# Optimization experiments

Measured on AMD Instinct MI355X. Metric: run time of the kernel, lower is better.

The kernel has to match this reference:

```python
import jax, jax.numpy as jnp
import numpy as np

SHIFT = 1  # shift_direction fixed to +1 (original picks +/-1 randomly at init)


def setup_inputs() -> dict:
    key = jax.random.key(0)
    kx, kw = jax.random.split(key)
    x = jax.random.normal(kx, (128, 128, 56, 56), dtype=jnp.float32)  # (N, C, H, W)
    w = jax.random.normal(kw, (32, 3, 128), dtype=jnp.float32)        # (out_ch, ktap, in_ch)
    return {"x": x, "w": w}


def reference(x, w):
    # roll along W (original dim 3), then 1x3 conv along W with SAME padding,
    # then roll the output along H (original dim 2).
    xr = jnp.roll(x, SHIFT, axis=3)
    # einsum 'nkmilo,jki->njmlo' == correlation: y[n,j,h,w] = sum_{k,i} xr[n,i,h,w+k-1] * w[j,k,i]
    kernel = jnp.transpose(w, (0, 2, 1))[:, :, None, :]  # (O=32, I=128, kh=1, kw=3)
    y = jax.lax.conv_general_dilated(
        xr, kernel,
        window_strides=(1, 1),
        padding=((0, 0), (1, 1)),
        dimension_numbers=("NCHW", "OIHW", "NCHW"),
    )  # (128, 32, 56, 56)
    return jnp.roll(y, SHIFT, axis=2)
```

## Files before the change

### kernel.cpp

```cpp
#include <hip/hip_runtime.h>
#include <stddef.h>


#define C_IN   128
#define C_OUT  32
#define HH     56
#define WW     56
#define HW     3136
#define KTOT   384
#define WSTRIDE 392
#define XSTRIDE 136
#define XROWSZ (57 * XSTRIDE)

typedef short bf16x8 __attribute__((ext_vector_type(8)));
typedef float f32x4  __attribute__((ext_vector_type(4)));
typedef float f32x4v __attribute__((ext_vector_type(4)));

static __device__ __forceinline__ unsigned short f2b(float f) {
    unsigned u = __builtin_bit_cast(unsigned, f);
    unsigned r = u + 0x7FFFu + ((u >> 16) & 1u);
    return (unsigned short)(r >> 16);
}

static __device__ __forceinline__ unsigned pk2(float lo, float hi) {
    unsigned r;
    asm("v_cvt_pk_bf16_f32 %0, %1, %2" : "=v"(r) : "v"(lo), "v"(hi));
    return r;
}

__global__ void pack_w_kernel(const float* __restrict__ w, unsigned short* __restrict__ ws) {
    int idx = blockIdx.x * 256 + threadIdx.x;
    if (idx < C_OUT * WSTRIDE) {
        int j = idx / WSTRIDE;
        int r = idx % WSTRIDE;
        ws[idx] = f2b(r < KTOT ? w[j * KTOT + r] : 0.0f);
    }
}

__global__ __launch_bounds__(512, 4)
void conv_mfma_kernel(const float* __restrict__ x, const unsigned short* __restrict__ ws,
                      float* __restrict__ out) {
    const int bid  = blockIdx.x;
    const int n    = bid / (HH / 4);
    const int h0   = (bid % (HH / 4)) * 4;
    const int tid  = threadIdx.x;
    const int lane = tid & 63;
    const int grp  = tid >> 6;

    __shared__ __align__(16) unsigned short XT[4 * XROWSZ];

    if (tid < 68) {
        int r = tid / 17, off = (tid % 17) * 8;
        *(uint4*)&XT[r * XROWSZ + WW * XSTRIDE + off] = make_uint4(0, 0, 0, 0);
    }

    const float* xb = x + (size_t)n * (C_IN * HW);

    {
        const int q  = lane;
        const int r  = q / 14;
        const int c4 = q % 14;
        const int hs = (h0 + 55 + r) % HH;
        const float* src0 = xb + (size_t)hs * WW + c4 * 4;
        unsigned short* dstc = &XT[r * XROWSZ + (c4 * 4) * XSTRIDE];
        if (q < WW) {
#pragma unroll
            for (int p = 0; p < 2; ++p) {
                const int ch0 = p * 64 + grp * 8;
                f32x4v v[8];
#pragma unroll
                for (int cc = 0; cc < 8; ++cc)
                    v[cc] = *(const f32x4v*)(src0 + (size_t)(ch0 + cc) * HW);
#pragma unroll
                for (int vc = 0; vc < 4; ++vc) {
                    uint4 w128;
                    w128.x = pk2(v[0][vc], v[1][vc]);
                    w128.y = pk2(v[2][vc], v[3][vc]);
                    w128.z = pk2(v[4][vc], v[5][vc]);
                    w128.w = pk2(v[6][vc], v[7][vc]);
                    *(uint4*)(dstc + vc * XSTRIDE + ch0) = w128;
                }
            }
        }
    }
    __syncthreads();

    const int l15 = lane & 15;
    const int kb  = (lane >> 4) * 8;
    const int rr  = grp >> 1;
    const int hf  = grp & 1;
    const unsigned short* Xr = &XT[rr * XROWSZ];

    const unsigned short* bp[2][3];
#pragma unroll
    for (int ct2 = 0; ct2 < 2; ++ct2) {
        const int nn = (hf * 2 + ct2) * 16 + l15;
        const int cc0 = (nn >= 1 && nn <= 55) ? (nn + 54) % WW : WW;
        const int cc1 = (nn <= 55) ? (nn + 55) % WW : WW;
        const int cc2 = (nn <= 54) ? nn : WW;
        bp[ct2][0] = Xr + cc0 * XSTRIDE + kb;
        bp[ct2][1] = Xr + cc1 * XSTRIDE + kb;
        bp[ct2][2] = Xr + cc2 * XSTRIDE + kb;
    }

    const unsigned short* wp = ws + l15 * WSTRIDE + kb;

    f32x4 acc[2][2];
#pragma unroll
    for (int ct2 = 0; ct2 < 2; ++ct2) {
        acc[ct2][0] = (f32x4){0.f, 0.f, 0.f, 0.f};
        acc[ct2][1] = (f32x4){0.f, 0.f, 0.f, 0.f};
    }

#pragma unroll
    for (int c = 0; c < 12; ++c) {
        const int tap = c >> 2;
        const int ib  = (c & 3) * 32;
        bf16x8 A0 = *(const bf16x8*)(wp + c * 32);
        bf16x8 A1 = *(const bf16x8*)(wp + 16 * WSTRIDE + c * 32);
#pragma unroll
        for (int ct2 = 0; ct2 < 2; ++ct2) {
            bf16x8 B = *(const bf16x8*)(bp[ct2][tap] + ib);
            acc[ct2][0] = __builtin_amdgcn_mfma_f32_16x16x32_bf16(A0, B, acc[ct2][0], 0, 0, 0);
            acc[ct2][1] = __builtin_amdgcn_mfma_f32_16x16x32_bf16(A1, B, acc[ct2][1], 0, 0, 0);
        }
    }

    {
        const int h  = h0 + rr;
        const int j0 = (lane >> 4) * 4;
        float* ob = out + (size_t)n * (C_OUT * HW) + (size_t)h * WW;
#pragma unroll
        for (int ct2 = 0; ct2 < 2; ++ct2) {
            const int nn = (hf * 2 + ct2) * 16 + l15;
            if (nn < WW) {
#pragma unroll
                for (int r = 0; r < 4; ++r) {
                    ob[(size_t)(j0 + r) * HW + nn]      = acc[ct2][0][r];
                    ob[(size_t)(j0 + r + 16) * HW + nn] = acc[ct2][1][r];
                }
            }
        }
    }
}

extern "C" void kernel_launch(void* const* d_in, const int* in_sizes, int n_in,
                              void* d_out, int out_size, void* d_ws, size_t ws_size,
                              hipStream_t stream) {
    const float* x = (const float*)d_in[0];
    const float* w = (const float*)d_in[1];
    float* out = (float*)d_out;
    unsigned short* ws = (unsigned short*)d_ws;

    pack_w_kernel<<<(C_OUT * WSTRIDE + 255) / 256, 256, 0, stream>>>(w, ws);
    conv_mfma_kernel<<<dim3(128 * (HH / 4)), dim3(512), 0, stream>>>(x, ws, out);
}
```

Baseline: 303.0 us.

## Make conv kernel persistent per image half with double-buffered LDS prefetch

Replaces the grid of one block per four-row tile with 256 blocks of 1024 threads, each looping over seven row tiles of one half image. Global loads for the next tile are issued before the MFMA work on the current tile and written into a second LDS buffer afterwards. Packed weights are copied into LDS once per block instead of being read from global memory per tile. In exchange, only 256 blocks run on a device with many CUs, and the large LDS footprint lowers occupancy, which may leave the device underused for this memory-bound kernel.

```diff
diff --git a/kernel.cpp b/kernel.cpp
--- a/kernel.cpp
+++ b/kernel.cpp
@@ -11,10 +11,10 @@
 #define WSTRIDE 392
 #define XSTRIDE 136
 #define XROWSZ (57 * XSTRIDE)
+#define NT     7
 
 typedef short bf16x8 __attribute__((ext_vector_type(8)));
 typedef float f32x4  __attribute__((ext_vector_type(4)));
-typedef float f32x4v __attribute__((ext_vector_type(4)));
 
 static __device__ __forceinline__ unsigned short f2b(float f) {
     unsigned u = __builtin_bit_cast(unsigned, f);
@@ -37,40 +37,114 @@
     }
 }
 
-__global__ __launch_bounds__(512, 4)
+__global__ __launch_bounds__(1024, 4)
 void conv_mfma_kernel(const float* __restrict__ x, const unsigned short* __restrict__ ws,
                       float* __restrict__ out) {
     const int bid  = blockIdx.x;
-    const int n    = bid / (HH / 4);
-    const int h0   = (bid % (HH / 4)) * 4;
+    const int n    = bid >> 1;
+    const int half = bid & 1;
     const int tid  = threadIdx.x;
     const int lane = tid & 63;
     const int grp  = tid >> 6;
 
-    __shared__ __align__(16) unsigned short XT[4 * XROWSZ];
+    __shared__ __align__(16) unsigned short SH[8 * XROWSZ + C_OUT * WSTRIDE];
+    unsigned short* const WSL = SH + 8 * XROWSZ;
 
-    if (tid < 68) {
-        int r = tid / 17, off = (tid % 17) * 8;
-        *(uint4*)&XT[r * XROWSZ + WW * XSTRIDE + off] = make_uint4(0, 0, 0, 0);
+    if (tid < 136) {
+        int b = tid / 68, r2 = (tid % 68) / 17, off = (tid % 17) * 8;
+        *(uint4*)&SH[(b * 4 + r2) * XROWSZ + WW * XSTRIDE + off] = make_uint4(0, 0, 0, 0);
     }
+    for (int i = tid; i < (C_OUT * WSTRIDE) / 8; i += 1024)
+        ((uint4*)WSL)[i] = ((const uint4*)ws)[i];
 
-    const float* xb = x + (size_t)n * (C_IN * HW);
+    const int q   = lane;
+    const int rs  = q / 14;
+    const int c4  = q % 14;
+    const int ch0 = grp * 8;
+    const bool act = (q < WW);
+    const float* xb = x + (size_t)n * (C_IN * HW) + (size_t)ch0 * HW + (size_t)(c4 * 4);
+
+    const int l15 = lane & 15;
+    const int kb  = (lane >> 4) * 8;
+    const int rr  = grp >> 2;
+    const int qt  = grp & 3;
+    const int nn  = qt * 16 + l15;
+    int cco[3];
+    cco[0] = (nn >= 1 && nn <= 55) ? (nn + 54) % WW : WW;
+    cco[1] = (nn <= 55) ? (nn + 55) % WW : WW;
+    cco[2] = (nn <= 54) ? nn : WW;
+    const int bo0 = rr * XROWSZ + cco[0] * XSTRIDE + kb;
+    const int bo1 = rr * XROWSZ + cco[1] * XSTRIDE + kb;
+    const int bo2 = rr * XROWSZ + cco[2] * XSTRIDE + kb;
+    const unsigned short* wp = WSL + l15 * WSTRIDE + kb;
+    const int j0 = (lane >> 4) * 4;
+    float* const outb = out + (size_t)n * (C_OUT * HW);
 
     {
-        const int q  = lane;
-        const int r  = q / 14;
-        const int c4 = q % 14;
-        const int hs = (h0 + 55 + r) % HH;
-        const float* src0 = xb + (size_t)hs * WW + c4 * 4;
-        unsigned short* dstc = &XT[r * XROWSZ + (c4 * 4) * XSTRIDE];
-        if (q < WW) {
+        const int h0 = (half * NT) * 4;
+        const int hs = (h0 + 55 + rs) % HH;
+        f32x4 v[8];
+        if (act) {
+            const float* s0 = xb + (size_t)hs * WW;
 #pragma unroll
-            for (int p = 0; p < 2; ++p) {
-                const int ch0 = p * 64 + grp * 8;
-                f32x4v v[8];
+            for (int cc = 0; cc < 8; ++cc)
+                v[cc] = *(const f32x4*)(s0 + (size_t)cc * HW);
+            unsigned short* dstc = SH + rs * XROWSZ + (c4 * 4) * XSTRIDE + ch0;
 #pragma unroll
-                for (int cc = 0; cc < 8; ++cc)
-                    v[cc] = *(const f32x4v*)(src0 + (size_t)(ch0 + cc) * HW);
+            for (int vc = 0; vc < 4; ++vc) {
+                uint4 w128;
+                w128.x = pk2(v[0][vc], v[1][vc]);
+                w128.y = pk2(v[2][vc], v[3][vc]);
+                w128.z = pk2(v[4][vc], v[5][vc]);
+                w128.w = pk2(v[6][vc], v[7][vc]);
+                *(uint4*)(dstc + vc * XSTRIDE) = w128;
+            }
+        }
+    }
+    __syncthreads();
+
+    for (int t = 0; t < NT; ++t) {
+        f32x4 v[8];
+        if (t + 1 < NT && act) {
+            const int h0n = (half * NT + t + 1) * 4;
+            const int hsn = (h0n + 55 + rs) % HH;
+            const float* s0 = xb + (size_t)hsn * WW;
+#pragma unroll
+            for (int cc = 0; cc < 8; ++cc)
+                v[cc] = *(const f32x4*)(s0 + (size_t)cc * HW);
+        }
+
+        const unsigned short* Xb = SH + (t & 1) * 4 * XROWSZ;
+        f32x4 acc0 = (f32x4){0.f, 0.f, 0.f, 0.f};
+        f32x4 acc1 = (f32x4){0.f, 0.f, 0.f, 0.f};
+#pragma unroll
+        for (int c = 0; c < 12; ++c) {
+            const int tap = c >> 2;
+            const int ib  = (c & 3) * 32;
+            bf16x8 A0 = *(const bf16x8*)(wp + c * 32);
+            bf16x8 A1 = *(const bf16x8*)(wp + 16 * WSTRIDE + c * 32);
+            const unsigned short* bpt = Xb + (tap == 0 ? bo0 : tap == 1 ? bo1 : bo2);
+            bf16x8 B = *(const bf16x8*)(bpt + ib);
+            acc0 = __builtin_amdgcn_mfma_f32_16x16x32_bf16(A0, B, acc0, 0, 0, 0);
+            acc1 = __builtin_amdgcn_mfma_f32_16x16x32_bf16(A1, B, acc1, 0, 0, 0);
+        }
+
+        {
+            const int h = (half * NT + t) * 4 + rr;
+            float* ob = outb + (size_t)h * WW;
+            if (nn < WW) {
+#pragma unroll
+                for (int r4 = 0; r4 < 4; ++r4) {
+                    ob[(size_t)(j0 + r4) * HW + nn]      = acc0[r4];
+                    ob[(size_t)(j0 + r4 + 16) * HW + nn] = acc1[r4];
+                }
+            }
+        }
+
+        if (t + 1 < NT) {
+            if (act) {
+                unsigned short* dstc = SH + ((t + 1) & 1) * 4 * XROWSZ
+                                     + rs * XROWSZ + (c4 * 4) * XSTRIDE + ch0;
 #pragma unroll
                 for (int vc = 0; vc < 4; ++vc) {
                     uint4 w128;
@@ -78,68 +152,10 @@
                     w128.y = pk2(v[2][vc], v[3][vc]);
                     w128.z = pk2(v[4][vc], v[5][vc]);
                     w128.w = pk2(v[6][vc], v[7][vc]);
-                    *(uint4*)(dstc + vc * XSTRIDE + ch0) = w128;
+                    *(uint4*)(dstc + vc * XSTRIDE) = w128;
                 }
             }
-        }
-    }
-    __syncthreads();
-
-    const int l15 = lane & 15;
-    const int kb  = (lane >> 4) * 8;
-    const int rr  = grp >> 1;
-    const int hf  = grp & 1;
-    const unsigned short* Xr = &XT[rr * XROWSZ];
-
-    const unsigned short* bp[2][3];
-#pragma unroll
-    for (int ct2 = 0; ct2 < 2; ++ct2) {
-        const int nn = (hf * 2 + ct2) * 16 + l15;
-        const int cc0 = (nn >= 1 && nn <= 55) ? (nn + 54) % WW : WW;
-        const int cc1 = (nn <= 55) ? (nn + 55) % WW : WW;
-        const int cc2 = (nn <= 54) ? nn : WW;
-        bp[ct2][0] = Xr + cc0 * XSTRIDE + kb;
-        bp[ct2][1] = Xr + cc1 * XSTRIDE + kb;
-        bp[ct2][2] = Xr + cc2 * XSTRIDE + kb;
-    }
-
-    const unsigned short* wp = ws + l15 * WSTRIDE + kb;
-
-    f32x4 acc[2][2];
-#pragma unroll
-    for (int ct2 = 0; ct2 < 2; ++ct2) {
-        acc[ct2][0] = (f32x4){0.f, 0.f, 0.f, 0.f};
-        acc[ct2][1] = (f32x4){0.f, 0.f, 0.f, 0.f};
-    }
-
-#pragma unroll
-    for (int c = 0; c < 12; ++c) {
-        const int tap = c >> 2;
-        const int ib  = (c & 3) * 32;
-        bf16x8 A0 = *(const bf16x8*)(wp + c * 32);
-        bf16x8 A1 = *(const bf16x8*)(wp + 16 * WSTRIDE + c * 32);
-#pragma unroll
-        for (int ct2 = 0; ct2 < 2; ++ct2) {
-            bf16x8 B = *(const bf16x8*)(bp[ct2][tap] + ib);
-            acc[ct2][0] = __builtin_amdgcn_mfma_f32_16x16x32_bf16(A0, B, acc[ct2][0], 0, 0, 0);
-            acc[ct2][1] = __builtin_amdgcn_mfma_f32_16x16x32_bf16(A1, B, acc[ct2][1], 0, 0, 0);
-        }
-    }
-
-    {
-        const int h  = h0 + rr;
-        const int j0 = (lane >> 4) * 4;
-        float* ob = out + (size_t)n * (C_OUT * HW) + (size_t)h * WW;
-#pragma unroll
-        for (int ct2 = 0; ct2 < 2; ++ct2) {
-            const int nn = (hf * 2 + ct2) * 16 + l15;
-            if (nn < WW) {
-#pragma unroll
-                for (int r = 0; r < 4; ++r) {
-                    ob[(size_t)(j0 + r) * HW + nn]      = acc[ct2][0][r];
-                    ob[(size_t)(j0 + r + 16) * HW + nn] = acc[ct2][1][r];
-                }
-            }
+            __syncthreads();
         }
     }
 }
@@ -153,5 +169,5 @@
     unsigned short* ws = (unsigned short*)d_ws;
 
     pack_w_kernel<<<(C_OUT * WSTRIDE + 255) / 256, 256, 0, stream>>>(w, ws);
-    conv_mfma_kernel<<<dim3(128 * (HH / 4)), dim3(512), 0, stream>>>(x, ws, out);
+    conv_mfma_kernel<<<dim3(256), dim3(1024), 0, stream>>>(x, ws, out);
 }
```

Result: no change. 306.1 us (+1.0%).
